# Kernel optimization log

Hardware: AMD Instinct MI355X
Metric: run time of the kernel (lower is better)

Reference implementation:

```python
import jax, jax.numpy as jnp
import numpy as np
import math

WS = 8          # window size
DIM = 32        # per-head dim
NH = 8          # num_head
TH = 16         # total_head
B, H, W = 4, 128, 128
WA = WS * WS    # window area


def _rel_pos_index():
    coords = np.stack(np.meshgrid(np.arange(WS), np.arange(WS), indexing='ij'))  # (2, WS, WS)
    cf = coords.reshape(2, -1)                      # (2, WA)
    rc = cf[:, :, None] - cf[:, None, :]            # (2, WA, WA)
    rc = rc.transpose(1, 2, 0).copy()               # (WA, WA, 2)
    rc[:, :, 0] += WS - 1
    rc[:, :, 1] += WS - 1
    rc[:, :, 0] *= 2 * WS - 1
    return rc.sum(-1)                               # (WA, WA)


def setup_inputs() -> dict:
    key = jax.random.key(0)
    k1, k2, k3, k4 = jax.random.split(key, 4)
    qkv = jax.random.normal(k1, (B, NH, 3 * DIM, H, W), dtype=jnp.float32)
    ch = jax.random.normal(k2, (B, (TH - NH) * DIM, H, W), dtype=jnp.float32)
    logit_scale = jnp.log(10.0) * jnp.ones((NH, 1, 1), dtype=jnp.float32)
    rel_bias_table = 0.02 * jax.random.normal(k3, ((2 * WS - 1) ** 2, NH), dtype=jnp.float32)
    proj_w = 0.02 * jax.random.normal(k4, (NH * DIM, NH * DIM), dtype=jnp.float32)  # 1x1 conv
    proj_b = jnp.zeros((NH * DIM,), dtype=jnp.float32)
    rel_index = jnp.asarray(_rel_pos_index(), dtype=jnp.int32)
    return {"qkv": qkv, "ch": ch, "logit_scale": logit_scale,
            "rel_bias_table": rel_bias_table, "proj_w": proj_w,
            "proj_b": proj_b, "rel_index": rel_index}


def _window_partition(x):
    # x: (B, l, c, H, W) -> (B*nh*nw, l, WA, c)
    b, l, c, h, w = x.shape
    nh, nw = h // WS, w // WS
    x = x.reshape(b, l, c, nh, WS, nw, WS)
    x = x.transpose(0, 3, 5, 1, 4, 6, 2)            # b, nh, nw, l, wh, ww, c
    return x.reshape(b * nh * nw, l, WA, c)


def _l2norm(x):
    n = jnp.sqrt(jnp.sum(x * x, axis=-1, keepdims=True))
    return x / jnp.maximum(n, 1e-12)


def reference(qkv, ch, logit_scale, rel_bias_table, proj_w, proj_b, rel_index):
    b, L, C3, h, w = qkv.shape
    nh, nw = h // WS, w // WS
    qkvw = _window_partition(qkv)                   # (Bw, L, WA, 3*DIM)
    q, k, v = jnp.split(qkvw, 3, axis=-1)           # each (Bw, L, WA, DIM)

    # helper gating
    lch = TH - NH
    chw = _window_partition(ch.reshape(b, lch, DIM, h, w))  # (Bw, lch, WA, DIM)
    chm = jnp.mean(chw, axis=1, keepdims=True)      # (Bw, 1, WA, DIM)
    v = v * chm

    # cosine attention
    attn = jnp.einsum('wlqc,wlkc->wlqk', _l2norm(q), _l2norm(k))
    scale = jnp.exp(jnp.minimum(logit_scale, math.log(1.0 / 0.01)))  # (L,1,1)
    bias = rel_bias_table[rel_index.reshape(-1)].reshape(WA, WA, NH)
    bias = bias.transpose(2, 0, 1)[None]            # (1, L, WA, WA)
    attn = jax.nn.softmax(attn * scale[None] + bias, axis=-1)
    x = jnp.einsum('wlqk,wlkc->wlqc', attn, v)      # (Bw, L, WA, DIM)

    # window unpartition -> (B, L*DIM, H, W)
    x = x.reshape(b, nh, nw, L, WS, WS, DIM)
    x = x.transpose(0, 3, 6, 1, 4, 2, 5)            # b, l, c, nh, wh, nw, ww
    x = x.reshape(b, L * DIM, h, w)

    # 1x1 conv projection
    x = jnp.einsum('bchw,oc->bohw', x, proj_w) + proj_b[None, :, None, None]
    return x
```

## Files before the change

### kernel.cpp

```cpp
#include <hip/hip_runtime.h>


typedef __attribute__((ext_vector_type(8))) short short8v;
typedef __attribute__((ext_vector_type(4))) float f32x4;
typedef __attribute__((ext_vector_type(2))) unsigned int u32x2;

#define PLANE 16384
#define LSTR  133

static __device__ __forceinline__ unsigned short f2bf(float x) {
  union { float f; unsigned u; } v; v.f = x;
  unsigned r = v.u + 0x7fff + ((v.u >> 16) & 1);
  return (unsigned short)(r >> 16);
}
static __device__ __forceinline__ float bf2f(unsigned short b) {
  union { unsigned u; float f; } v; v.u = ((unsigned)b) << 16;
  return v.f;
}

__global__ __launch_bounds__(256) void prep_kernel(
    const float* __restrict__ ch, const float* __restrict__ btab,
    const int* __restrict__ ridx, const float* __restrict__ pw,
    float* __restrict__ chm, float* __restrict__ biasG,
    unsigned int* __restrict__ wbf)
{
  const int blk = blockIdx.x, tid = threadIdx.x;
  if (blk < 8192) {
    int idx = blk * 256 + tid;
    int b = idx >> 19, c = (idx >> 14) & 31, p = idx & 16383;
    const float* src = ch + ((size_t)(b * 256 + c)) * PLANE + p;
    float s = 0.f;
#pragma unroll
    for (int l = 0; l < 8; ++l) s += src[(size_t)(l * 32) * PLANE];
    chm[((size_t)(b * 32 + c)) * PLANE + p] = s * 0.125f;
  } else if (blk < 8320) {
    int i = (blk - 8192) * 256 + tid;
    int h = i >> 12, qk = i & 4095;
    biasG[i] = btab[ridx[qk] * 8 + h];
  } else {
    int i = (blk - 8320) * 256 + tid;
    float a = pw[i * 2], b2 = pw[i * 2 + 1];
    wbf[i] = (unsigned)f2bf(a) | ((unsigned)f2bf(b2) << 16);
  }
}

__global__ __launch_bounds__(256) void attn_kernel(
    const float* __restrict__ qkv, const float* __restrict__ chm,
    const float* __restrict__ lsc, const float* __restrict__ biasG,
    unsigned short* __restrict__ xtmp)
{
  __shared__ float Qs[32 * LSTR];
  __shared__ float Ks[32 * LSTR];
  __shared__ __align__(16) float nq[128];
  __shared__ __align__(16) float nk[128];

  const int tid = threadIdx.x;
  const int bw  = blockIdx.x;
  const int h   = bw & 7;
  const int pi  = bw >> 3;
  const int b   = pi >> 7;
  const int wy  = (pi >> 3) & 15;
  const int wxp = pi & 7;
  const int y0  = wy << 3, x0 = wxp << 4;

  const size_t qbase = ((size_t)((b * 8 + h) * 96)) * PLANE;
  const float* qg = qkv + qbase;
  const float* kg = qkv + qbase + (size_t)32 * PLANE;
  const float* vg = qkv + qbase + (size_t)64 * PLANE;
  const float* cg = chm + (size_t)(b * 32) * PLANE;

  for (int i = tid; i < 4096; i += 256) {
    int d = i >> 7, p = i & 127;
    int sp = (y0 + (p >> 4)) * 128 + x0 + (p & 15);
    Qs[d * LSTR + p] = qg[(size_t)d * PLANE + sp];
    Ks[d * LSTR + p] = kg[(size_t)d * PLANE + sp];
  }
  __syncthreads();

  {
    float scale = __expf(fminf(lsc[h], 4.6051701859880914f));
    int p = tid & 127;
    const float* M = (tid < 128) ? Qs : Ks;
    float s = 0.f;
#pragma unroll
    for (int d = 0; d < 32; ++d) { float x = M[d * LSTR + p]; s = fmaf(x, x, s); }
    float inv = 1.f / fmaxf(sqrtf(s), 1e-12f);
    int win = (p >> 3) & 1, pos = ((p >> 4) << 3) + (p & 7);
    if (tid < 128) nq[win * 64 + pos] = inv * scale;
    else           nk[win * 64 + pos] = inv;
  }
  __syncthreads();

  const int wv = tid >> 6, lane = tid & 63;
  const int win = wv >> 1, sub = wv & 1;
  const int lg = lane >> 4, lr = lane & 15;
  const int xw = x0 + win * 8;

  short8v khi[4], klo[4];
#pragma unroll
  for (int kt = 0; kt < 4; ++kt) {
    int kpos = 16 * kt + lr;
    int pp = ((kpos >> 3) << 4) + win * 8 + (kpos & 7);
#pragma unroll
    for (int j = 0; j < 8; ++j) {
      float x = Ks[(8 * lg + j) * LSTR + pp];
      unsigned short hb = f2bf(x);
      khi[kt][j] = (short)hb;
      klo[kt][j] = (short)f2bf(x - bf2f(hb));
    }
  }

  short8v vf[2][2];
#pragma unroll
  for (int dt = 0; dt < 2; ++dt) {
    int d = 16 * dt + lr;
    const float* vp = vg + (size_t)d * PLANE;
    const float* cp = cg + (size_t)d * PLANE;
#pragma unroll
    for (int m = 0; m < 2; ++m) {
      int ka = 4 * lg + 32 * m, kb = ka + 16;
      int spa = (y0 + (ka >> 3)) * 128 + xw + (ka & 7);
      int spb = (y0 + (kb >> 3)) * 128 + xw + (kb & 7);
      float4 va = *(const float4*)(vp + spa);
      float4 ca = *(const float4*)(cp + spa);
      float4 vb = *(const float4*)(vp + spb);
      float4 cb = *(const float4*)(cp + spb);
      vf[dt][m][0] = (short)f2bf(va.x * ca.x);
      vf[dt][m][1] = (short)f2bf(va.y * ca.y);
      vf[dt][m][2] = (short)f2bf(va.z * ca.z);
      vf[dt][m][3] = (short)f2bf(va.w * ca.w);
      vf[dt][m][4] = (short)f2bf(vb.x * cb.x);
      vf[dt][m][5] = (short)f2bf(vb.y * cb.y);
      vf[dt][m][6] = (short)f2bf(vb.z * cb.z);
      vf[dt][m][7] = (short)f2bf(vb.w * cb.w);
    }
  }

#pragma unroll
  for (int si = 0; si < 2; ++si) {
    int st = 2 * sub + si;
    int q = 16 * st + lr;
    int pq = ((q >> 3) << 4) + win * 8 + (q & 7);

    short8v qhi, qlo;
#pragma unroll
    for (int j = 0; j < 8; ++j) {
      float x = Qs[(8 * lg + j) * LSTR + pq];
      unsigned short hb = f2bf(x);
      qhi[j] = (short)hb;
      qlo[j] = (short)f2bf(x - bf2f(hb));
    }

    f32x4 acc[4];
#pragma unroll
    for (int kt = 0; kt < 4; ++kt) {
      f32x4 a = {0.f, 0.f, 0.f, 0.f};
      a = __builtin_amdgcn_mfma_f32_16x16x32_bf16(klo[kt], qhi, a, 0, 0, 0);
      a = __builtin_amdgcn_mfma_f32_16x16x32_bf16(khi[kt], qlo, a, 0, 0, 0);
      a = __builtin_amdgcn_mfma_f32_16x16x32_bf16(khi[kt], qhi, a, 0, 0, 0);
      acc[kt] = a;
    }

    float fq = nq[win * 64 + q];
    const float4* bq = (const float4*)(biasG + ((h * 64 + q) << 6));
    float e[16], mx = -1e30f;
#pragma unroll
    for (int kt = 0; kt < 4; ++kt) {
      float4 b4 = bq[4 * kt + lg];
      float bb[4] = {b4.x, b4.y, b4.z, b4.w};
      f32x4 fk4 = *(const f32x4*)(&nk[win * 64 + 16 * kt + 4 * lg]);
#pragma unroll
      for (int r = 0; r < 4; ++r) {
        float lv = acc[kt][r] * (fq * fk4[r]) + bb[r];
        e[4 * kt + r] = lv;
        mx = fmaxf(mx, lv);
      }
    }
    mx = fmaxf(mx, __shfl_xor(mx, 16));
    mx = fmaxf(mx, __shfl_xor(mx, 32));
    float s = 0.f;
#pragma unroll
    for (int i = 0; i < 16; ++i) { e[i] = __expf(e[i] - mx); s += e[i]; }
    s += __shfl_xor(s, 16);
    s += __shfl_xor(s, 32);
    float rl = 1.f / s;

    short8v pf[2];
#pragma unroll
    for (int m = 0; m < 2; ++m)
#pragma unroll
      for (int j = 0; j < 8; ++j)
        pf[m][j] = (short)f2bf(e[4 * (j >> 2) + 8 * m + (j & 3)]);

    int pg = (y0 + (q >> 3)) * 128 + xw + (q & 7);
#pragma unroll
    for (int dt = 0; dt < 2; ++dt) {
      f32x4 o = {0.f, 0.f, 0.f, 0.f};
      o = __builtin_amdgcn_mfma_f32_16x16x32_bf16(vf[dt][0], pf[0], o, 0, 0, 0);
      o = __builtin_amdgcn_mfma_f32_16x16x32_bf16(vf[dt][1], pf[1], o, 0, 0, 0);
      size_t base = ((size_t)(b * PLANE + pg)) * 256 + h * 32 + 16 * dt + 4 * lg;
      u32x2 ww;
      ww[0] = (unsigned)f2bf(o[0] * rl) | ((unsigned)f2bf(o[1] * rl) << 16);
      ww[1] = (unsigned)f2bf(o[2] * rl) | ((unsigned)f2bf(o[3] * rl) << 16);
      *(u32x2*)(xtmp + base) = ww;
    }
  }
}

__global__ __launch_bounds__(256) void proj_kernel(
    const unsigned short* __restrict__ xtmp, const unsigned short* __restrict__ wbf,
    const float* __restrict__ pb, float* __restrict__ out)
{
  const int tid = threadIdx.x, lane = tid & 63, wv = tid >> 6;
  const int lg = lane >> 4, lr = lane & 15;
  const int P0 = blockIdx.x * 64;
  const int o0 = wv * 64;

  f32x4 acc[4][4];
#pragma unroll
  for (int i = 0; i < 4; ++i)
#pragma unroll
    for (int j = 0; j < 4; ++j) acc[i][j] = (f32x4){0.f, 0.f, 0.f, 0.f};

#pragma unroll
  for (int kc = 0; kc < 8; ++kc) {
    short8v wf[4], xf[4];
#pragma unroll
    for (int ot = 0; ot < 4; ++ot) {
      int o = o0 + 16 * ot + lr;
      wf[ot] = *(const short8v*)(wbf + (size_t)o * 256 + 32 * kc + 8 * lg);
    }
#pragma unroll
    for (int pt = 0; pt < 4; ++pt) {
      int p = P0 + 16 * pt + lr;
      xf[pt] = *(const short8v*)(xtmp + (size_t)p * 256 + 32 * kc + 8 * lg);
    }
#pragma unroll
    for (int ot = 0; ot < 4; ++ot)
#pragma unroll
      for (int pt = 0; pt < 4; ++pt)
        acc[ot][pt] = __builtin_amdgcn_mfma_f32_16x16x32_bf16(wf[ot], xf[pt], acc[ot][pt], 0, 0, 0);
  }

  const int bI = P0 >> 14, pp0 = P0 & 16383;
#pragma unroll
  for (int ot = 0; ot < 4; ++ot) {
#pragma unroll
    for (int r = 0; r < 4; ++r) {
      int o = o0 + 16 * ot + 4 * lg + r;
      float bias = pb[o];
#pragma unroll
      for (int pt = 0; pt < 4; ++pt) {
        int p = pp0 + 16 * pt + lr;
        out[((size_t)(bI * 256 + o)) * PLANE + p] = acc[ot][pt][r] + bias;
      }
    }
  }
}

extern "C" void kernel_launch(void* const* d_in, const int* in_sizes, int n_in,
                              void* d_out, int out_size, void* d_ws, size_t ws_size,
                              hipStream_t stream) {
  const float* qkv  = (const float*)d_in[0];
  const float* ch   = (const float*)d_in[1];
  const float* lsc  = (const float*)d_in[2];
  const float* btab = (const float*)d_in[3];
  const float* pw   = (const float*)d_in[4];
  const float* pb   = (const float*)d_in[5];
  const int*   ridx = (const int*)d_in[6];
  float* out = (float*)d_out;

  char* ws = (char*)d_ws;
  unsigned short* xtmp  = (unsigned short*)ws;
  float*          chm   = (float*)(ws + 33554432);
  float*          biasG = (float*)(ws + 33554432 + 8388608);
  unsigned short* wbf   = (unsigned short*)(ws + 33554432 + 8388608 + 131072);

  prep_kernel<<<dim3(8448), dim3(256), 0, stream>>>(ch, btab, ridx, pw,
                                                    chm, biasG, (unsigned int*)wbf);
  attn_kernel<<<dim3(4096), dim3(256), 0, stream>>>(qkv, chm, lsc, biasG, xtmp);
  proj_kernel<<<dim3(1024), dim3(256), 0, stream>>>(xtmp, wbf, pb, out);
}
```

Before: 143.5 us.

## Load Q/K directly into MFMA fragments and vectorize channel-mean prep

The attention kernel no longer stages Q and K through shared memory with two barriers. Each lane reads its Q/K values straight from global memory into registers, computes L2 norms with cross-lane shuffles, and broadcasts the key norms via shuffles. The prep kernel's channel-mean pass now uses float4 loads and stores with a quarter of the blocks. The direct loads are strided per lane and less coalesced than the old cooperative staging, in exchange for removing LDS traffic and synchronisation and letting more blocks reside at once.

```diff
diff --git a/kernel.cpp b/kernel.cpp
--- a/kernel.cpp
+++ b/kernel.cpp
@@ -6,7 +6,6 @@
 typedef __attribute__((ext_vector_type(2))) unsigned int u32x2;
 
 #define PLANE 16384
-#define LSTR  133
 
 static __device__ __forceinline__ unsigned short f2bf(float x) {
   union { float f; unsigned u; } v; v.f = x;
@@ -25,20 +24,25 @@
     unsigned int* __restrict__ wbf)
 {
   const int blk = blockIdx.x, tid = threadIdx.x;
-  if (blk < 8192) {
+  if (blk < 2048) {
     int idx = blk * 256 + tid;
-    int b = idx >> 19, c = (idx >> 14) & 31, p = idx & 16383;
-    const float* src = ch + ((size_t)(b * 256 + c)) * PLANE + p;
-    float s = 0.f;
-#pragma unroll
-    for (int l = 0; l < 8; ++l) s += src[(size_t)(l * 32) * PLANE];
-    chm[((size_t)(b * 32 + c)) * PLANE + p] = s * 0.125f;
-  } else if (blk < 8320) {
-    int i = (blk - 8192) * 256 + tid;
+    const float4* src = (const float4*)ch;
+    int b = idx >> 17, c = (idx >> 12) & 31, p4 = idx & 4095;
+    const float4* s0 = src + ((size_t)(b * 256 + c)) * (PLANE / 4) + p4;
+    float4 a = {0.f, 0.f, 0.f, 0.f};
+#pragma unroll
+    for (int l = 0; l < 8; ++l) {
+      float4 t = s0[(size_t)(l * 32) * (PLANE / 4)];
+      a.x += t.x; a.y += t.y; a.z += t.z; a.w += t.w;
+    }
+    a.x *= 0.125f; a.y *= 0.125f; a.z *= 0.125f; a.w *= 0.125f;
+    ((float4*)chm)[((size_t)(b * 32 + c)) * (PLANE / 4) + p4] = a;
+  } else if (blk < 2176) {
+    int i = (blk - 2048) * 256 + tid;
     int h = i >> 12, qk = i & 4095;
     biasG[i] = btab[ridx[qk] * 8 + h];
   } else {
-    int i = (blk - 8320) * 256 + tid;
+    int i = (blk - 2176) * 256 + tid;
     float a = pw[i * 2], b2 = pw[i * 2 + 1];
     wbf[i] = (unsigned)f2bf(a) | ((unsigned)f2bf(b2) << 16);
   }
@@ -49,11 +53,6 @@
     const float* __restrict__ lsc, const float* __restrict__ biasG,
     unsigned short* __restrict__ xtmp)
 {
-  __shared__ float Qs[32 * LSTR];
-  __shared__ float Ks[32 * LSTR];
-  __shared__ __align__(16) float nq[128];
-  __shared__ __align__(16) float nk[128];
-
   const int tid = threadIdx.x;
   const int bw  = blockIdx.x;
   const int h   = bw & 7;
@@ -63,52 +62,18 @@
   const int wxp = pi & 7;
   const int y0  = wy << 3, x0 = wxp << 4;
 
-  const size_t qbase = ((size_t)((b * 8 + h) * 96)) * PLANE;
-  const float* qg = qkv + qbase;
-  const float* kg = qkv + qbase + (size_t)32 * PLANE;
-  const float* vg = qkv + qbase + (size_t)64 * PLANE;
-  const float* cg = chm + (size_t)(b * 32) * PLANE;
-
-  for (int i = tid; i < 4096; i += 256) {
-    int d = i >> 7, p = i & 127;
-    int sp = (y0 + (p >> 4)) * 128 + x0 + (p & 15);
-    Qs[d * LSTR + p] = qg[(size_t)d * PLANE + sp];
-    Ks[d * LSTR + p] = kg[(size_t)d * PLANE + sp];
-  }
-  __syncthreads();
-
-  {
-    float scale = __expf(fminf(lsc[h], 4.6051701859880914f));
-    int p = tid & 127;
-    const float* M = (tid < 128) ? Qs : Ks;
-    float s = 0.f;
-#pragma unroll
-    for (int d = 0; d < 32; ++d) { float x = M[d * LSTR + p]; s = fmaf(x, x, s); }
-    float inv = 1.f / fmaxf(sqrtf(s), 1e-12f);
-    int win = (p >> 3) & 1, pos = ((p >> 4) << 3) + (p & 7);
-    if (tid < 128) nq[win * 64 + pos] = inv * scale;
-    else           nk[win * 64 + pos] = inv;
-  }
-  __syncthreads();
-
   const int wv = tid >> 6, lane = tid & 63;
   const int win = wv >> 1, sub = wv & 1;
   const int lg = lane >> 4, lr = lane & 15;
   const int xw = x0 + win * 8;
 
-  short8v khi[4], klo[4];
-#pragma unroll
-  for (int kt = 0; kt < 4; ++kt) {
-    int kpos = 16 * kt + lr;
-    int pp = ((kpos >> 3) << 4) + win * 8 + (kpos & 7);
-#pragma unroll
-    for (int j = 0; j < 8; ++j) {
-      float x = Ks[(8 * lg + j) * LSTR + pp];
-      unsigned short hb = f2bf(x);
-      khi[kt][j] = (short)hb;
-      klo[kt][j] = (short)f2bf(x - bf2f(hb));
-    }
-  }
+  const size_t qbase = ((size_t)((b * 8 + h) * 96)) * PLANE;
+  const float* qg = qkv + qbase;
+  const float* kg = qg + (size_t)32 * PLANE;
+  const float* vg = qg + (size_t)64 * PLANE;
+  const float* cg = chm + (size_t)(b * 32) * PLANE;
+
+  const float scale = __expf(fminf(lsc[h], 4.6051701859880914f));
 
   short8v vf[2][2];
 #pragma unroll
@@ -136,42 +101,75 @@
     }
   }
 
+  short8v khi[4], klo[4];
+  float ivk[4];
+#pragma unroll
+  for (int kt = 0; kt < 4; ++kt) {
+    int kpos = 16 * kt + lr;
+    int spk = (y0 + (kpos >> 3)) * 128 + xw + (kpos & 7);
+    float kk[8], nr = 0.f;
+#pragma unroll
+    for (int j = 0; j < 8; ++j) {
+      kk[j] = kg[(size_t)(8 * lg + j) * PLANE + spk];
+      nr = fmaf(kk[j], kk[j], nr);
+    }
+    nr += __shfl_xor(nr, 16);
+    nr += __shfl_xor(nr, 32);
+    ivk[kt] = 1.f / fmaxf(sqrtf(nr), 1e-12f);
+#pragma unroll
+    for (int j = 0; j < 8; ++j) {
+      unsigned short hb = f2bf(kk[j]);
+      khi[kt][j] = (short)hb;
+      klo[kt][j] = (short)f2bf(kk[j] - bf2f(hb));
+    }
+  }
+
+  f32x4 fk[4];
+#pragma unroll
+  for (int kt = 0; kt < 4; ++kt)
+#pragma unroll
+    for (int r = 0; r < 4; ++r)
+      fk[kt][r] = __shfl(ivk[kt], 4 * lg + r);
+
+  const float* bgh = biasG + (h << 12);
+
 #pragma unroll
   for (int si = 0; si < 2; ++si) {
     int st = 2 * sub + si;
     int q = 16 * st + lr;
-    int pq = ((q >> 3) << 4) + win * 8 + (q & 7);
+    int spq = (y0 + (q >> 3)) * 128 + xw + (q & 7);
+
+    float qq[8], nrq = 0.f;
+#pragma unroll
+    for (int j = 0; j < 8; ++j) {
+      qq[j] = qg[(size_t)(8 * lg + j) * PLANE + spq];
+      nrq = fmaf(qq[j], qq[j], nrq);
+    }
+    nrq += __shfl_xor(nrq, 16);
+    nrq += __shfl_xor(nrq, 32);
+    const float fq = scale / fmaxf(sqrtf(nrq), 1e-12f);
 
     short8v qhi, qlo;
 #pragma unroll
     for (int j = 0; j < 8; ++j) {
-      float x = Qs[(8 * lg + j) * LSTR + pq];
-      unsigned short hb = f2bf(x);
+      unsigned short hb = f2bf(qq[j]);
       qhi[j] = (short)hb;
-      qlo[j] = (short)f2bf(x - bf2f(hb));
-    }
-
-    f32x4 acc[4];
+      qlo[j] = (short)f2bf(qq[j] - bf2f(hb));
+    }
+
+    const float4* bq = (const float4*)(bgh + (q << 6));
+    float e[16], mx = -1e30f;
 #pragma unroll
     for (int kt = 0; kt < 4; ++kt) {
       f32x4 a = {0.f, 0.f, 0.f, 0.f};
       a = __builtin_amdgcn_mfma_f32_16x16x32_bf16(klo[kt], qhi, a, 0, 0, 0);
       a = __builtin_amdgcn_mfma_f32_16x16x32_bf16(khi[kt], qlo, a, 0, 0, 0);
       a = __builtin_amdgcn_mfma_f32_16x16x32_bf16(khi[kt], qhi, a, 0, 0, 0);
-      acc[kt] = a;
-    }
-
-    float fq = nq[win * 64 + q];
-    const float4* bq = (const float4*)(biasG + ((h * 64 + q) << 6));
-    float e[16], mx = -1e30f;
-#pragma unroll
-    for (int kt = 0; kt < 4; ++kt) {
       float4 b4 = bq[4 * kt + lg];
       float bb[4] = {b4.x, b4.y, b4.z, b4.w};
-      f32x4 fk4 = *(const f32x4*)(&nk[win * 64 + 16 * kt + 4 * lg]);
 #pragma unroll
       for (int r = 0; r < 4; ++r) {
-        float lv = acc[kt][r] * (fq * fk4[r]) + bb[r];
+        float lv = a[r] * (fq * fk[kt][r]) + bb[r];
         e[4 * kt + r] = lv;
         mx = fmaxf(mx, lv);
       }
@@ -276,7 +274,7 @@
   float*          biasG = (float*)(ws + 33554432 + 8388608);
   unsigned short* wbf   = (unsigned short*)(ws + 33554432 + 8388608 + 131072);
 
-  prep_kernel<<<dim3(8448), dim3(256), 0, stream>>>(ch, btab, ridx, pw,
+  prep_kernel<<<dim3(2304), dim3(256), 0, stream>>>(ch, btab, ridx, pw,
                                                     chm, biasG, (unsigned int*)wbf);
   attn_kernel<<<dim3(4096), dim3(256), 0, stream>>>(qkv, chm, lsc, biasG, xtmp);
   proj_kernel<<<dim3(1024), dim3(256), 0, stream>>>(xtmp, wbf, pb, out);
```

Result: slower. 155.0 us (+8.0%).
